# Kernel tuning notes

Measured on AMD Instinct MI355X. Metric: run time of the kernel, lower is better.

Reference implementation:

```python
import jax, jax.numpy as jnp
import numpy as np

HEADS = 2
HID = 128
IN_DIM = 128
OUT_DIM = 1
N_NODES = 50000
NEG_SLOPE = 0.2  # PyG GATConv default
EPS = 1e-16


def setup_inputs() -> dict:
    key = jax.random.key(0)
    ks = jax.random.split(key, 16)
    N, E = N_NODES, 800000
    x = jax.random.normal(ks[0], (N, IN_DIM), dtype=jnp.float32)
    edge_index = jax.random.randint(ks[1], (2, E), 0, N, dtype=jnp.int32)
    s = 0.1
    # GATConv 1: in=128 -> heads=2, out=128 per head
    W1 = jax.random.normal(ks[2], (IN_DIM, HEADS * HID), dtype=jnp.float32) * s
    a_src1 = jax.random.normal(ks[3], (HEADS, HID), dtype=jnp.float32) * s
    a_dst1 = jax.random.normal(ks[4], (HEADS, HID), dtype=jnp.float32) * s
    b1 = jnp.zeros((HEADS * HID,), dtype=jnp.float32)
    # GATConv 2: in=256 -> heads=2, out=128 per head
    W2 = jax.random.normal(ks[5], (HEADS * HID, HEADS * HID), dtype=jnp.float32) * s
    a_src2 = jax.random.normal(ks[6], (HEADS, HID), dtype=jnp.float32) * s
    a_dst2 = jax.random.normal(ks[7], (HEADS, HID), dtype=jnp.float32) * s
    b2 = jnp.zeros((HEADS * HID,), dtype=jnp.float32)
    # post_mp: Linear(256,128) -> Dropout -> Linear(128,1)
    Wp1 = jax.random.normal(ks[8], (HEADS * HID, HID), dtype=jnp.float32) * s
    bp1 = jnp.zeros((HID,), dtype=jnp.float32)
    Wp2 = jax.random.normal(ks[9], (HID, OUT_DIM), dtype=jnp.float32) * s
    bp2 = jnp.zeros((OUT_DIM,), dtype=jnp.float32)
    return {"x": x, "edge_index": edge_index,
            "W1": W1, "a_src1": a_src1, "a_dst1": a_dst1, "b1": b1,
            "W2": W2, "a_src2": a_src2, "a_dst2": a_dst2, "b2": b2,
            "Wp1": Wp1, "bp1": bp1, "Wp2": Wp2, "bp2": bp2}


def gat_conv(x, src, dst, W, a_src, a_dst, b, num_nodes):
    """PyG-style GATConv (concat=True). src/dst already include self-loops."""
    N = num_nodes
    h = (x @ W).reshape(N, HEADS, HID)                        # [N,H,C]
    alpha_s = jnp.einsum('nhc,hc->nh', h, a_src)              # [N,H]
    alpha_d = jnp.einsum('nhc,hc->nh', h, a_dst)              # [N,H]
    e = jax.nn.leaky_relu(alpha_s[src] + alpha_d[dst], NEG_SLOPE)  # [E,H]
    # segment softmax over destination node
    emax = jax.ops.segment_max(e, dst, num_segments=N)        # [N,H]
    emax = jnp.where(jnp.isfinite(emax), emax, 0.0)
    w = jnp.exp(e - emax[dst])                                # [E,H]
    denom = jax.ops.segment_sum(w, dst, num_segments=N)       # [N,H]
    alpha = w / (denom[dst] + EPS)                            # [E,H]
    out = jax.ops.segment_sum(h[src] * alpha[:, :, None], dst, num_segments=N)
    return out.reshape(N, HEADS * HID) + b


def reference(x, edge_index, W1, a_src1, a_dst1, b1, W2, a_src2, a_dst2, b2,
              Wp1, bp1, Wp2, bp2):
    N = x.shape[0]
    loops = jnp.arange(N, dtype=edge_index.dtype)
    src = jnp.concatenate([edge_index[0], loops])
    dst = jnp.concatenate([edge_index[1], loops])
    h = gat_conv(x, src, dst, W1, a_src1, a_dst1, b1, N)
    h = jax.nn.relu(h)  # dropout is identity in eval mode
    h = gat_conv(h, src, dst, W2, a_src2, a_dst2, b2, N)
    h = jax.nn.relu(h)
    h = h @ Wp1 + bp1
    h = h @ Wp2 + bp2
    return jax.nn.sigmoid(h)
```

## Files before the change

kernel.cpp:

```cpp
#include <hip/hip_runtime.h>

#define HID 128
#define C2 256
#define NEG 0.2f

typedef __bf16 v8bf __attribute__((ext_vector_type(8)));
typedef float  v4f  __attribute__((ext_vector_type(4)));
typedef float  v2f  __attribute__((ext_vector_type(2)));
typedef unsigned short us8 __attribute__((ext_vector_type(8)));

__device__ __forceinline__ float bf2f(unsigned short u) {
    union { float f; unsigned int i; } v; v.i = ((unsigned int)u) << 16; return v.f;
}
__device__ __forceinline__ unsigned short f2bf(float f) {
    union { float f; unsigned int i; } v; v.f = f;
    unsigned int r = v.i + 0x7FFFu + ((v.i >> 16) & 1u);
    return (unsigned short)(r >> 16);
}
__device__ __forceinline__ float lrelu(float x) { return x > 0.f ? x : NEG * x; }

__device__ __forceinline__ void packB_body(const float* __restrict__ W,
                                           unsigned short* __restrict__ out,
                                           int K, int N, int idx) {
    int ksteps = K >> 5;
    int total = (N >> 4) * ksteps * 64;
    if (idx >= total) return;
    int lane = idx & 63;
    int rest = idx >> 6;
    int tt = rest / ksteps, k0 = rest - tt * ksteps;
    int n = (tt >> 3) * 128 + (lane & 15) * 8 + (tt & 7);
    int kb = k0 * 32 + (lane >> 4) * 8;
    us8 v;
#pragma unroll
    for (int j = 0; j < 8; ++j) v[j] = f2bf(W[(size_t)(kb + j) * N + n]);
    *(us8*)(out + (size_t)idx * 8) = v;
}

__global__ __launch_bounds__(256) void prep_kernel(const float* __restrict__ W1, unsigned short* W1p,
                                                   const float* __restrict__ W2, unsigned short* W2p,
                                                   const float* __restrict__ Wp1, unsigned short* Wp1p,
                                                   const int* __restrict__ ei, int* __restrict__ cnt,
                                                   int* __restrict__ rank, int E,
                                                   int b1, int b2, int b3) {
    int b = blockIdx.x;
    if (b < b1) { packB_body(W1, W1p, HID, C2, b * 256 + threadIdx.x); return; }
    b -= b1;
    if (b < b2) { packB_body(W2, W2p, C2, C2, b * 256 + threadIdx.x); return; }
    b -= b2;
    if (b < b3) { packB_body(Wp1, Wp1p, C2, HID, b * 256 + threadIdx.x); return; }
    b -= b3;
    int i = b * 256 + threadIdx.x;
    if (i >= E) return;
    int d = ei[E + i];
    rank[i] = atomicAdd(&cnt[d], 1);
}

__global__ __launch_bounds__(256) void scanA(const int* __restrict__ cnt, int* __restrict__ rs,
                                             int* __restrict__ part, int N) {
    __shared__ int s[256];
    int t = threadIdx.x, i = blockIdx.x * 256 + t;
    int v = (i < N) ? cnt[i] : 0;
    s[t] = v; __syncthreads();
    for (int off = 1; off < 256; off <<= 1) {
        int x = (t >= off) ? s[t - off] : 0;
        __syncthreads();
        s[t] += x;
        __syncthreads();
    }
    if (i < N) rs[i] = s[t] - v;
    if (t == 255) part[blockIdx.x] = s[255];
}

__global__ __launch_bounds__(256) void scanB(int* __restrict__ part, int n) {
    __shared__ int s[256];
    int t = threadIdx.x;
    int v = (t < n) ? part[t] : 0;
    s[t] = v; __syncthreads();
    for (int off = 1; off < 256; off <<= 1) {
        int x = (t >= off) ? s[t - off] : 0;
        __syncthreads();
        s[t] += x;
        __syncthreads();
    }
    if (t < n) part[t] = s[t] - v;
}

__global__ void scanC(int* __restrict__ rs, const int* __restrict__ part, int N, int E) {
    int i = blockIdx.x * 256 + threadIdx.x;
    if (i < N) rs[i] += part[blockIdx.x];
    if (i == 0) rs[N] = E;
}

template<bool AFP32, int G>
__global__ __launch_bounds__(256) void gemm_alpha(const void* __restrict__ Av,
                                                  const unsigned short* __restrict__ Bp,
                                                  const float* __restrict__ asrc,
                                                  const float* __restrict__ adst,
                                                  float* __restrict__ asd,
                                                  unsigned char* __restrict__ C,
                                                  int M, int N, int K, int gemmBlocks,
                                                  const int* __restrict__ ei,
                                                  const int* __restrict__ rs,
                                                  const int* __restrict__ rank,
                                                  int* __restrict__ csr, int E) {
    if (blockIdx.x >= gemmBlocks) {
        int i = (blockIdx.x - gemmBlocks) * 256 + threadIdx.x;
        if (i < E) {
            int s = ei[i], d = ei[E + i];
            csr[rs[d] + rank[i]] = s;
        }
        return;
    }
    int ksteps = K >> 5;
    int ngrp = N >> 7;
    int mtiles = M >> 4;
    int w = (blockIdx.x << 2) + (threadIdx.x >> 6);
    int groups = (mtiles + G - 1) / G;
    int mp = w / ngrp, g = w - mp * ngrp;
    if (mp >= groups) return;
    int lane = threadIdx.x & 63;
    int l16 = lane & 15, quad = lane >> 4;
    int mt0 = mp * G;

    int mrow[G];
#pragma unroll
    for (int gi = 0; gi < G; ++gi) {
        int mt = mt0 + gi;
        mrow[gi] = (mt < mtiles ? mt : mtiles - 1) * 16 + l16;
    }

    const unsigned short* Bf = Bp + ((size_t)(g * 8) * ksteps << 9) + lane * 8;
    v4f acc[G][8];
#pragma unroll
    for (int gi = 0; gi < G; ++gi)
#pragma unroll
        for (int t = 0; t < 8; ++t) acc[gi][t] = (v4f){0, 0, 0, 0};

    for (int k0 = 0; k0 < ksteps; ++k0) {
        v8bf a[G];
        if (AFP32) {
            const float* A = (const float*)Av;
#pragma unroll
            for (int gi = 0; gi < G; ++gi) {
                const float* p = A + (size_t)mrow[gi] * K + k0 * 32 + quad * 8;
                float4 u0 = *(const float4*)p, u1 = *(const float4*)(p + 4);
                a[gi][0]=(__bf16)u0.x; a[gi][1]=(__bf16)u0.y; a[gi][2]=(__bf16)u0.z; a[gi][3]=(__bf16)u0.w;
                a[gi][4]=(__bf16)u1.x; a[gi][5]=(__bf16)u1.y; a[gi][6]=(__bf16)u1.z; a[gi][7]=(__bf16)u1.w;
            }
        } else {
            const unsigned short* A = (const unsigned short*)Av;
#pragma unroll
            for (int gi = 0; gi < G; ++gi)
                a[gi] = *(const v8bf*)(A + (size_t)mrow[gi] * K + k0 * 32 + quad * 8);
        }
#pragma unroll
        for (int t = 0; t < 8; ++t) {
            v8bf bfr = *(const v8bf*)(Bf + ((size_t)(t * ksteps + k0) << 9));
#pragma unroll
            for (int gi = 0; gi < G; ++gi)
                acc[gi][t] = __builtin_amdgcn_mfma_f32_16x16x32_bf16(a[gi], bfr, acc[gi][t], 0, 0, 0);
        }
    }

    int n0 = g << 7;
    int cb = n0 + l16 * 8;
    float sv[8], dv[8];
#pragma unroll
    for (int t = 0; t < 8; ++t) {
        sv[t] = asrc[cb + t];
        dv[t] = adst[cb + t];
    }
#pragma unroll
    for (int gi = 0; gi < G; ++gi) {
        int mt = mt0 + gi;
        if (mt >= mtiles) break;
        int row0 = mt * 16 + quad * 4;
#pragma unroll
        for (int r = 0; r < 4; ++r) {
            float sa = 0.f, sd = 0.f;
#pragma unroll
            for (int t = 0; t < 8; ++t) {
                sa += acc[gi][t][r] * sv[t];
                sd += acc[gi][t][r] * dv[t];
            }
            unsigned int w0 = __builtin_amdgcn_cvt_pk_fp8_f32(acc[gi][0][r], acc[gi][1][r], 0, false);
            w0 = __builtin_amdgcn_cvt_pk_fp8_f32(acc[gi][2][r], acc[gi][3][r], w0, true);
            unsigned int w1 = __builtin_amdgcn_cvt_pk_fp8_f32(acc[gi][4][r], acc[gi][5][r], 0, false);
            w1 = __builtin_amdgcn_cvt_pk_fp8_f32(acc[gi][6][r], acc[gi][7][r], w1, true);
            *(uint2*)(C + (size_t)(row0 + r) * N + cb) = (uint2){w0, w1};
#pragma unroll
            for (int off = 8; off; off >>= 1) {
                sa += __shfl_xor(sa, off);
                sd += __shfl_xor(sd, off);
            }
            if (l16 == 0) {
                int row = row0 + r;
                asd[(size_t)row * 4 + g]     = sa;
                asd[(size_t)row * 4 + 2 + g] = sd;
            }
        }
    }
}

__global__ __launch_bounds__(256) void agg_kernel(const int* __restrict__ rs,
                                                  const int* __restrict__ csr,
                                                  const unsigned char* __restrict__ h,
                                                  const float* __restrict__ asd,
                                                  const float* __restrict__ bias,
                                                  unsigned short* __restrict__ out, int N) {
    int d = blockIdx.x * 4 + (threadIdx.x >> 6);
    if (d >= N) return;
    int lane = threadIdx.x & 63;
    int beg = rs[d], end = rs[d + 1];
    int e2 = lane >> 5;
    int sub = lane & 31;
    int head = sub >> 4;
    float adh = asd[(size_t)d * 4 + 2 + head];
    int cbase = sub * 8;
    const unsigned char* hc = h + cbase;
    v2f a01 = {0, 0}, a23 = {0, 0}, a45 = {0, 0}, a67 = {0, 0};
    float den = 0.f;
#pragma unroll 2
    for (int i = beg; i < end; i += 2) {
        int ei = i + e2;
        bool valid = ei < end;
        int s = csr[valid ? ei : end - 1];
        float e = lrelu(asd[(size_t)s * 4 + head] + adh);
        float wgt = valid ? __expf(e) : 0.f;
        den += wgt;
        uint2 u = *(const uint2*)(hc + (size_t)s * C2);
        v2f w2 = {wgt, wgt};
        a01 += w2 * __builtin_amdgcn_cvt_pk_f32_fp8(u.x, false);
        a23 += w2 * __builtin_amdgcn_cvt_pk_f32_fp8(u.x, true);
        a45 += w2 * __builtin_amdgcn_cvt_pk_f32_fp8(u.y, false);
        a67 += w2 * __builtin_amdgcn_cvt_pk_f32_fp8(u.y, true);
    }
    float a[8] = {a01.x, a01.y, a23.x, a23.y, a45.x, a45.y, a67.x, a67.y};
#pragma unroll
    for (int j = 0; j < 8; ++j) a[j] += __shfl_xor(a[j], 32);
    den += __shfl_xor(den, 32);
    if (e2 == 0) {
        float wS = __expf(lrelu(asd[(size_t)d * 4 + head] + adh));
        uint2 u = *(const uint2*)(hc + (size_t)d * C2);
        v2f p0 = __builtin_amdgcn_cvt_pk_f32_fp8(u.x, false);
        v2f p1 = __builtin_amdgcn_cvt_pk_f32_fp8(u.x, true);
        v2f p2 = __builtin_amdgcn_cvt_pk_f32_fp8(u.y, false);
        v2f p3 = __builtin_amdgcn_cvt_pk_f32_fp8(u.y, true);
        a[0] += wS * p0.x; a[1] += wS * p0.y;
        a[2] += wS * p1.x; a[3] += wS * p1.y;
        a[4] += wS * p2.x; a[5] += wS * p2.y;
        a[6] += wS * p3.x; a[7] += wS * p3.y;
        float rden = 1.f / (den + wS + 1e-16f);
        us8 o;
#pragma unroll
        for (int j = 0; j < 8; ++j) o[j] = f2bf(fmaxf(a[j] * rden + bias[cbase + j], 0.f));
        *(us8*)(out + (size_t)d * C2 + cbase) = o;
    }
}

template<int G>
__global__ __launch_bounds__(256) void gemm_final(const unsigned short* __restrict__ A,
                                                  const unsigned short* __restrict__ Bp,
                                                  const float* __restrict__ bp1,
                                                  const float* __restrict__ wp2,
                                                  const float* __restrict__ bp2,
                                                  float* __restrict__ out,
                                                  int M, int K) {
    int ksteps = K >> 5;
    int mtiles = M >> 4;
    int groups = (mtiles + G - 1) / G;
    int mp = (blockIdx.x << 2) + (threadIdx.x >> 6);
    if (mp >= groups) return;
    int lane = threadIdx.x & 63;
    int l16 = lane & 15, quad = lane >> 4;

    int mrow[G];
#pragma unroll
    for (int gi = 0; gi < G; ++gi) {
        int mt = mp * G + gi;
        mrow[gi] = (mt < mtiles ? mt : mtiles - 1) * 16 + l16;
    }

    const unsigned short* Bf = Bp + lane * 8;
    v4f acc[G][8];
#pragma unroll
    for (int gi = 0; gi < G; ++gi)
#pragma unroll
        for (int t = 0; t < 8; ++t) acc[gi][t] = (v4f){0, 0, 0, 0};
    for (int k0 = 0; k0 < ksteps; ++k0) {
        v8bf a[G];
#pragma unroll
        for (int gi = 0; gi < G; ++gi)
            a[gi] = *(const v8bf*)(A + (size_t)mrow[gi] * K + k0 * 32 + quad * 8);
#pragma unroll
        for (int t = 0; t < 8; ++t) {
            v8bf bfr = *(const v8bf*)(Bf + ((size_t)(t * ksteps + k0) << 9));
#pragma unroll
            for (int gi = 0; gi < G; ++gi)
                acc[gi][t] = __builtin_amdgcn_mfma_f32_16x16x32_bf16(a[gi], bfr, acc[gi][t], 0, 0, 0);
        }
    }
    int cb = l16 * 8;
    float wv8[8], bv[8];
#pragma unroll
    for (int t = 0; t < 8; ++t) {
        wv8[t] = wp2[cb + t];
        bv[t] = bp1[cb + t];
    }
    float bias2 = bp2[0];
#pragma unroll
    for (int gi = 0; gi < G; ++gi) {
        int mt = mp * G + gi;
        if (mt >= mtiles) break;
        int row0 = mt * 16 + quad * 4;
#pragma unroll
        for (int r = 0; r < 4; ++r) {
            float s = 0.f;
#pragma unroll
            for (int t = 0; t < 8; ++t) s += (acc[gi][t][r] + bv[t]) * wv8[t];
#pragma unroll
            for (int off = 8; off; off >>= 1) s += __shfl_xor(s, off);
            if (l16 == 0) {
                float xv = s + bias2;
                out[row0 + r] = 1.f / (1.f + __expf(-xv));
            }
        }
    }
}

extern "C" void kernel_launch(void* const* d_in, const int* in_sizes, int n_in,
                              void* d_out, int out_size, void* d_ws, size_t ws_size,
                              hipStream_t stream) {
    const float* x   = (const float*)d_in[0];
    const int*   ei  = (const int*)d_in[1];
    const float* W1  = (const float*)d_in[2];
    const float* as1 = (const float*)d_in[3];
    const float* ad1 = (const float*)d_in[4];
    const float* b1  = (const float*)d_in[5];
    const float* W2  = (const float*)d_in[6];
    const float* as2 = (const float*)d_in[7];
    const float* ad2 = (const float*)d_in[8];
    const float* b2  = (const float*)d_in[9];
    const float* Wp1 = (const float*)d_in[10];
    const float* bp1 = (const float*)d_in[11];
    const float* Wp2 = (const float*)d_in[12];
    const float* bp2 = (const float*)d_in[13];
    float* out = (float*)d_out;

    int NN = in_sizes[0] / HID;
    int E  = in_sizes[1] / 2;

    char* ws = (char*)d_ws;
    size_t off = 0;
    auto alloc = [&](size_t bytes) -> char* {
        char* p = ws + off;
        off += (bytes + 255) & ~(size_t)255;
        return p;
    };
    unsigned char*  bufH = (unsigned char*)alloc((size_t)NN * C2);
    unsigned short* bufO = (unsigned short*)alloc((size_t)NN * C2 * 2);
    float* asd = (float*)alloc((size_t)NN * 4 * sizeof(float));
    int* rs    = (int*)alloc((size_t)(NN + 1) * 4);
    int* cnt   = (int*)alloc((size_t)NN * 4);
    int* rank  = (int*)alloc((size_t)E * 4);
    int* csr   = (int*)alloc((size_t)E * 4);
    int* part  = (int*)alloc(1024);
    unsigned short* W1p  = (unsigned short*)alloc((size_t)HID * C2 * 2);
    unsigned short* W2p  = (unsigned short*)alloc((size_t)C2 * C2 * 2);
    unsigned short* Wp1p = (unsigned short*)alloc((size_t)C2 * HID * 2);

    int nchunk = (NN + 255) / 256;
    int eblk   = (E + 255) / 256;

    int pb1 = (HID * C2 / 8 + 255) / 256;
    int pb2 = (C2 * C2 / 8 + 255) / 256;
    int pb3 = (C2 * HID / 8 + 255) / 256;
    hipMemsetAsync(cnt, 0, (size_t)NN * 4, stream);
    prep_kernel<<<pb1 + pb2 + pb3 + eblk, 256, 0, stream>>>(W1, W1p, W2, W2p, Wp1, Wp1p,
                                                            ei, cnt, rank, E, pb1, pb2, pb3);
    scanA<<<nchunk, 256, 0, stream>>>(cnt, rs, part, NN);
    scanB<<<1, 256, 0, stream>>>(part, nchunk);
    scanC<<<nchunk, 256, 0, stream>>>(rs, part, NN, E);

    const int G = 2;
    int mtiles = NN / 16;
    int groups = (mtiles + G - 1) / G;
    int gemmBlocks = (groups * 2 + 3) / 4;
    int aggGrid = (NN + 3) / 4;

    gemm_alpha<true, G><<<gemmBlocks + eblk, 256, 0, stream>>>(x, W1p, as1, ad1, asd, bufH,
                                                               NN, C2, HID, gemmBlocks,
                                                               ei, rs, rank, csr, E);
    agg_kernel<<<aggGrid, 256, 0, stream>>>(rs, csr, bufH, asd, b1, bufO, NN);
    gemm_alpha<false, G><<<gemmBlocks, 256, 0, stream>>>(bufO, W2p, as2, ad2, asd, bufH,
                                                         NN, C2, C2, gemmBlocks,
                                                         nullptr, nullptr, nullptr, nullptr, 0);
    agg_kernel<<<aggGrid, 256, 0, stream>>>(rs, csr, bufH, asd, b2, bufO, NN);
    gemm_final<G><<<(groups + 3) / 4, 256, 0, stream>>>(bufO, Wp1p, bp1, Wp2, bp2, out, NN, C2);
}
```

Before: 287.8 us.

## Widen aggregation to 16-byte loads over four edges and batch edge-sort work

Measured after the change: 295.3 us. +2.6%, slower.

```diff
diff --git a/kernel.cpp b/kernel.cpp
--- a/kernel.cpp
+++ b/kernel.cpp
@@ -49,10 +49,17 @@
     b -= b2;
     if (b < b3) { packB_body(Wp1, Wp1p, C2, HID, b * 256 + threadIdx.x); return; }
     b -= b3;
-    int i = b * 256 + threadIdx.x;
-    if (i >= E) return;
-    int d = ei[E + i];
-    rank[i] = atomicAdd(&cnt[d], 1);
+    int base = b * 1024 + threadIdx.x;
+    int d[4], ok = 0;
+#pragma unroll
+    for (int j = 0; j < 4; ++j) {
+        int i = base + j * 256;
+        if (i < E) { d[j] = ei[E + i]; ok = j + 1; }
+    }
+#pragma unroll
+    for (int j = 0; j < 4; ++j) {
+        if (j < ok) rank[base + j * 256] = atomicAdd(&cnt[d[j]], 1);
+    }
 }
 
 __global__ __launch_bounds__(256) void scanA(const int* __restrict__ cnt, int* __restrict__ rs,
@@ -104,10 +111,14 @@
                                                   const int* __restrict__ rank,
                                                   int* __restrict__ csr, int E) {
     if (blockIdx.x >= gemmBlocks) {
-        int i = (blockIdx.x - gemmBlocks) * 256 + threadIdx.x;
-        if (i < E) {
-            int s = ei[i], d = ei[E + i];
-            csr[rs[d] + rank[i]] = s;
+        int base = (blockIdx.x - gemmBlocks) * 1024 + threadIdx.x;
+#pragma unroll
+        for (int j = 0; j < 4; ++j) {
+            int i = base + j * 256;
+            if (i < E) {
+                int s = ei[i], d = ei[E + i];
+                __builtin_nontemporal_store(s, &csr[rs[d] + rank[i]]);
+            }
         }
         return;
     }
@@ -212,49 +223,65 @@
     if (d >= N) return;
     int lane = threadIdx.x & 63;
     int beg = rs[d], end = rs[d + 1];
-    int e2 = lane >> 5;
-    int sub = lane & 31;
-    int head = sub >> 4;
+    int e4 = lane >> 4;
+    int sub = lane & 15;
+    int head = sub >> 3;
     float adh = asd[(size_t)d * 4 + 2 + head];
-    int cbase = sub * 8;
+    int cbase = sub * 16;
     const unsigned char* hc = h + cbase;
-    v2f a01 = {0, 0}, a23 = {0, 0}, a45 = {0, 0}, a67 = {0, 0};
+    v2f a[8];
+#pragma unroll
+    for (int j = 0; j < 8; ++j) a[j] = (v2f){0, 0};
     float den = 0.f;
 #pragma unroll 2
-    for (int i = beg; i < end; i += 2) {
-        int ei = i + e2;
+    for (int i = beg; i < end; i += 4) {
+        int ei = i + e4;
         bool valid = ei < end;
         int s = csr[valid ? ei : end - 1];
         float e = lrelu(asd[(size_t)s * 4 + head] + adh);
         float wgt = valid ? __expf(e) : 0.f;
         den += wgt;
-        uint2 u = *(const uint2*)(hc + (size_t)s * C2);
+        uint4 u = *(const uint4*)(hc + (size_t)s * C2);
         v2f w2 = {wgt, wgt};
-        a01 += w2 * __builtin_amdgcn_cvt_pk_f32_fp8(u.x, false);
-        a23 += w2 * __builtin_amdgcn_cvt_pk_f32_fp8(u.x, true);
-        a45 += w2 * __builtin_amdgcn_cvt_pk_f32_fp8(u.y, false);
-        a67 += w2 * __builtin_amdgcn_cvt_pk_f32_fp8(u.y, true);
-    }
-    float a[8] = {a01.x, a01.y, a23.x, a23.y, a45.x, a45.y, a67.x, a67.y};
-#pragma unroll
-    for (int j = 0; j < 8; ++j) a[j] += __shfl_xor(a[j], 32);
+        a[0] += w2 * __builtin_amdgcn_cvt_pk_f32_fp8(u.x, false);
+        a[1] += w2 * __builtin_amdgcn_cvt_pk_f32_fp8(u.x, true);
+        a[2] += w2 * __builtin_amdgcn_cvt_pk_f32_fp8(u.y, false);
+        a[3] += w2 * __builtin_amdgcn_cvt_pk_f32_fp8(u.y, true);
+        a[4] += w2 * __builtin_amdgcn_cvt_pk_f32_fp8(u.z, false);
+        a[5] += w2 * __builtin_amdgcn_cvt_pk_f32_fp8(u.z, true);
+        a[6] += w2 * __builtin_amdgcn_cvt_pk_f32_fp8(u.w, false);
+        a[7] += w2 * __builtin_amdgcn_cvt_pk_f32_fp8(u.w, true);
+    }
+#pragma unroll
+    for (int j = 0; j < 8; ++j) {
+        a[j].x += __shfl_xor(a[j].x, 16); a[j].y += __shfl_xor(a[j].y, 16);
+        a[j].x += __shfl_xor(a[j].x, 32); a[j].y += __shfl_xor(a[j].y, 32);
+    }
+    den += __shfl_xor(den, 16);
     den += __shfl_xor(den, 32);
-    if (e2 == 0) {
+    if (e4 == 0) {
         float wS = __expf(lrelu(asd[(size_t)d * 4 + head] + adh));
-        uint2 u = *(const uint2*)(hc + (size_t)d * C2);
-        v2f p0 = __builtin_amdgcn_cvt_pk_f32_fp8(u.x, false);
-        v2f p1 = __builtin_amdgcn_cvt_pk_f32_fp8(u.x, true);
-        v2f p2 = __builtin_amdgcn_cvt_pk_f32_fp8(u.y, false);
-        v2f p3 = __builtin_amdgcn_cvt_pk_f32_fp8(u.y, true);
-        a[0] += wS * p0.x; a[1] += wS * p0.y;
-        a[2] += wS * p1.x; a[3] += wS * p1.y;
-        a[4] += wS * p2.x; a[5] += wS * p2.y;
-        a[6] += wS * p3.x; a[7] += wS * p3.y;
+        uint4 u = *(const uint4*)(hc + (size_t)d * C2);
+        v2f w2 = {wS, wS};
+        a[0] += w2 * __builtin_amdgcn_cvt_pk_f32_fp8(u.x, false);
+        a[1] += w2 * __builtin_amdgcn_cvt_pk_f32_fp8(u.x, true);
+        a[2] += w2 * __builtin_amdgcn_cvt_pk_f32_fp8(u.y, false);
+        a[3] += w2 * __builtin_amdgcn_cvt_pk_f32_fp8(u.y, true);
+        a[4] += w2 * __builtin_amdgcn_cvt_pk_f32_fp8(u.z, false);
+        a[5] += w2 * __builtin_amdgcn_cvt_pk_f32_fp8(u.z, true);
+        a[6] += w2 * __builtin_amdgcn_cvt_pk_f32_fp8(u.w, false);
+        a[7] += w2 * __builtin_amdgcn_cvt_pk_f32_fp8(u.w, true);
         float rden = 1.f / (den + wS + 1e-16f);
-        us8 o;
-#pragma unroll
-        for (int j = 0; j < 8; ++j) o[j] = f2bf(fmaxf(a[j] * rden + bias[cbase + j], 0.f));
-        *(us8*)(out + (size_t)d * C2 + cbase) = o;
+        us8 o0, o1;
+#pragma unroll
+        for (int j = 0; j < 4; ++j) {
+            o0[2*j]   = f2bf(fmaxf(a[j].x * rden + bias[cbase + 2*j],     0.f));
+            o0[2*j+1] = f2bf(fmaxf(a[j].y * rden + bias[cbase + 2*j + 1], 0.f));
+            o1[2*j]   = f2bf(fmaxf(a[4+j].x * rden + bias[cbase + 8 + 2*j],     0.f));
+            o1[2*j+1] = f2bf(fmaxf(a[4+j].y * rden + bias[cbase + 8 + 2*j + 1], 0.f));
+        }
+        *(us8*)(out + (size_t)d * C2 + cbase) = o0;
+        *(us8*)(out + (size_t)d * C2 + cbase + 8) = o1;
     }
 }
 
@@ -370,14 +397,14 @@
     unsigned short* Wp1p = (unsigned short*)alloc((size_t)C2 * HID * 2);
 
     int nchunk = (NN + 255) / 256;
-    int eblk   = (E + 255) / 256;
+    int eblk4  = (E + 1023) / 1024;
 
     int pb1 = (HID * C2 / 8 + 255) / 256;
     int pb2 = (C2 * C2 / 8 + 255) / 256;
     int pb3 = (C2 * HID / 8 + 255) / 256;
     hipMemsetAsync(cnt, 0, (size_t)NN * 4, stream);
-    prep_kernel<<<pb1 + pb2 + pb3 + eblk, 256, 0, stream>>>(W1, W1p, W2, W2p, Wp1, Wp1p,
-                                                            ei, cnt, rank, E, pb1, pb2, pb3);
+    prep_kernel<<<pb1 + pb2 + pb3 + eblk4, 256, 0, stream>>>(W1, W1p, W2, W2p, Wp1, Wp1p,
+                                                             ei, cnt, rank, E, pb1, pb2, pb3);
     scanA<<<nchunk, 256, 0, stream>>>(cnt, rs, part, NN);
     scanB<<<1, 256, 0, stream>>>(part, nchunk);
     scanC<<<nchunk, 256, 0, stream>>>(rs, part, NN, E);
@@ -388,9 +415,9 @@
     int gemmBlocks = (groups * 2 + 3) / 4;
     int aggGrid = (NN + 3) / 4;
 
-    gemm_alpha<true, G><<<gemmBlocks + eblk, 256, 0, stream>>>(x, W1p, as1, ad1, asd, bufH,
-                                                               NN, C2, HID, gemmBlocks,
-                                                               ei, rs, rank, csr, E);
+    gemm_alpha<true, G><<<gemmBlocks + eblk4, 256, 0, stream>>>(x, W1p, as1, ad1, asd, bufH,
+                                                                NN, C2, HID, gemmBlocks,
+                                                                ei, rs, rank, csr, E);
     agg_kernel<<<aggGrid, 256, 0, stream>>>(rs, csr, bufH, asd, b1, bufO, NN);
     gemm_alpha<false, G><<<gemmBlocks, 256, 0, stream>>>(bufO, W2p, as2, ad2, asd, bufH,
                                                          NN, C2, C2, gemmBlocks,
```
